# Kernel tuning notes

Hardware: AMD Instinct MI355X
Metric: run time of the kernel (lower is better)

## Reference

```python
import jax, jax.numpy as jnp
import numpy as np

BS, L, E, H, T, V = 1024, 128, 256, 512, 20, 1000


def setup_inputs() -> dict:
    key = jax.random.key(0)
    ks = jax.random.split(key, 16)
    s = 0.05
    msg = jax.random.randint(ks[0], (BS, T), 1, V + 1)
    M = jax.random.normal(ks[1], (BS, L, E), dtype=jnp.float32)
    input_mask = jax.random.randint(ks[2], (BS, L), 0, 2) == 1
    input_mask = input_mask.at[:, 0].set(False)  # guarantee >=1 unmasked slot
    lengths = jax.random.randint(ks[3], (BS,), 0, T + 1)
    emb = jax.random.normal(ks[4], (V + 1, E), dtype=jnp.float32) * s
    Wq = jax.random.normal(ks[5], (E, H), dtype=jnp.float32) * s   # query_projection
    bq = jnp.zeros((E,), dtype=jnp.float32)
    Wc = jax.random.normal(ks[6], (H, E + H), dtype=jnp.float32) * s  # attn_combine
    bc = jnp.zeros((H,), dtype=jnp.float32)
    W_ih = jax.random.normal(ks[7], (4 * H, E), dtype=jnp.float32) * s
    W_hh = jax.random.normal(ks[8], (4 * H, H), dtype=jnp.float32) * s
    b_ih = jnp.zeros((4 * H,), dtype=jnp.float32)
    b_hh = jnp.zeros((4 * H,), dtype=jnp.float32)
    return {"msg": msg, "M": M, "input_mask": input_mask, "lengths": lengths,
            "emb": emb, "Wq": Wq, "bq": bq, "Wc": Wc, "bc": bc,
            "W_ih": W_ih, "W_hh": W_hh, "b_ih": b_ih, "b_hh": b_hh}


def _attend(h, M, input_mask, Wq, bq, Wc, bc):
    # q=(bs,H) projected to key space (bs,E); scores over L objects
    pq = h @ Wq.T + bq                                   # (bs, E)
    scores = jnp.einsum('ble,be->bl', M, pq)             # (bs, L)
    scores = jnp.where(input_mask, -jnp.inf, scores)
    w = jax.nn.softmax(scores, axis=1)                   # (bs, L)
    applied = jnp.einsum('bl,ble->be', w, M)             # (bs, E)
    att_out = jnp.concatenate([applied, h], axis=1) @ Wc.T + bc  # (bs, H)
    return att_out, w


def _lstm_cell(x, h, c, W_ih, W_hh, b_ih, b_hh):
    gates = x @ W_ih.T + b_ih + h @ W_hh.T + b_hh        # (bs, 4H)
    i, f, g, o = jnp.split(gates, 4, axis=1)
    c_new = jax.nn.sigmoid(f) * c + jax.nn.sigmoid(i) * jnp.tanh(g)
    h_new = jax.nn.sigmoid(o) * jnp.tanh(c_new)
    return h_new, c_new


def reference(msg, M, input_mask, lengths, emb, Wq, bq, Wc, bc, W_ih, W_hh, b_ih, b_hh):
    bs = msg.shape[0]
    msg_embed = emb[msg]                                 # (bs, T, E)
    xs = jnp.swapaxes(msg_embed, 0, 1)                   # (T, bs, E)
    h0 = jnp.zeros((bs, H), dtype=M.dtype)
    c0 = jnp.zeros((bs, H), dtype=M.dtype)

    def step(carry, x):
        h, c = carry
        att_out, w = _attend(h, M, input_mask, Wq, bq, Wc, bc)
        h2, c2 = _lstm_cell(x, att_out, c, W_ih, W_hh, b_ih, b_hh)
        return (h2, c2), w

    (hT, _), ws = jax.lax.scan(step, (h0, c0), xs)       # ws: (T, bs, L)
    _, w_last = _attend(hT, M, input_mask, Wq, bq, Wc, bc)
    attn_weights = jnp.swapaxes(jnp.concatenate([ws, w_last[None]], axis=0), 0, 1)  # (bs, T+1, L)
    lengths_c = jnp.clip(lengths, 0, T)
    output = attn_weights[jnp.arange(bs), lengths_c]     # (bs, L)
    logits = jnp.zeros((bs,), dtype=M.dtype)
    entropy = logits
    return (output, logits, entropy)
```

## Files before the change

kernel.cpp:

```cpp
#include <hip/hip_runtime.h>
#include <math.h>

#define NB 1024
#define L_ 128
#define E_ 256
#define H_ 512
#define T_ 20
#define CH 32
#define NCH 4

typedef _Float16 h8 __attribute__((ext_vector_type(8)));
typedef float f4 __attribute__((ext_vector_type(4)));

__global__ __launch_bounds__(256) void detect_mask(const unsigned char* __restrict__ mask,
                                                   int* __restrict__ flag) {
    int i = blockIdx.x * 256 + threadIdx.x;
    if (mask[4 * i + 1] != 0) flag[0] = 1;
}

__global__ __launch_bounds__(256) void attend_part(
    const float* __restrict__ M, const unsigned char* __restrict__ maskB,
    const int* __restrict__ flag, const float* __restrict__ pq,
    float* __restrict__ pbuf,
    float* __restrict__ apart,
    float2* __restrict__ stats)
{
    const int s = blockIdx.x, b = blockIdx.y;
    const int tid = threadIdx.x;
    __shared__ float pq_s[E_];
    __shared__ float ps[CH];

    pq_s[tid] = pq[b * E_ + tid];
    __syncthreads();

    const int wave = tid >> 6, lane = tid & 63;
    const int r = lane >> 3, i = lane & 7;
    const int l = wave * 8 + r;
    const float* Mrow = M + ((size_t)b * L_ + s * CH + l) * E_;

    float acc = 0.f;
    #pragma unroll
    for (int j = 0; j < 8; ++j) {
        float4 mv = *reinterpret_cast<const float4*>(Mrow + i * 4 + j * 32);
        float4 pv = *reinterpret_cast<const float4*>(pq_s + i * 4 + j * 32);
        acc += mv.x * pv.x + mv.y * pv.y + mv.z * pv.z + mv.w * pv.w;
    }
    acc += __shfl_down(acc, 4, 64);
    acc += __shfl_down(acc, 2, 64);
    acc += __shfl_down(acc, 1, 64);

    __shared__ float sc[CH];
    if (i == 0) {
        const int lg = s * CH + l;
        int msk = flag[0] ? (int)maskB[b * L_ + lg] : ((const int*)maskB)[b * L_ + lg];
        sc[l] = msk ? -INFINITY : acc;
    }
    __syncthreads();

    if (wave == 0) {
        const float v = (lane < CH) ? sc[lane] : -INFINITY;
        float m = v;
        #pragma unroll
        for (int off = 32; off > 0; off >>= 1) m = fmaxf(m, __shfl_down(m, off, 64));
        m = __shfl(m, 0, 64);
        const float p = (lane < CH && !isinf(m)) ? __expf(v - m) : 0.f;
        float ss = p;
        #pragma unroll
        for (int off = 32; off > 0; off >>= 1) ss += __shfl_down(ss, off, 64);
        if (lane == 0) stats[b * NCH + s] = make_float2(m, ss);
        if (lane < CH) {
            ps[lane] = p;
            pbuf[b * L_ + s * CH + lane] = p;
        }
    }
    __syncthreads();

    const float* Mc = M + ((size_t)b * L_ + s * CH) * E_;
    float a = 0.f;
    #pragma unroll 8
    for (int l2 = 0; l2 < CH; ++l2) a += ps[l2] * Mc[l2 * E_ + tid];
    apart[((size_t)b * NCH + s) * E_ + tid] = a;
}

__global__ __launch_bounds__(256) void attend_combine(
    const float* __restrict__ pbuf, const float* __restrict__ apart,
    const float2* __restrict__ stats, const int* __restrict__ lengths,
    float* __restrict__ applied, float* __restrict__ out, int t, int writeApplied)
{
    const int b = blockIdx.x;
    const int tid = threadIdx.x;
    __shared__ float scale[NCH];
    __shared__ float zinv;

    if (tid == 0) {
        float m = -INFINITY;
        #pragma unroll
        for (int s = 0; s < NCH; ++s) m = fmaxf(m, stats[b * NCH + s].x);
        float Z = 0.f;
        #pragma unroll
        for (int s = 0; s < NCH; ++s) {
            const float2 st = stats[b * NCH + s];
            const float sc = isinf(st.x) ? 0.f : __expf(st.x - m);
            scale[s] = sc;
            Z += st.y * sc;
        }
        zinv = 1.f / Z;
    }
    __syncthreads();

    if (writeApplied) {
        float a = 0.f;
        #pragma unroll
        for (int s = 0; s < NCH; ++s)
            a += apart[((size_t)b * NCH + s) * E_ + tid] * scale[s];
        applied[b * E_ + tid] = a * zinv;
    }

    int lc = lengths[b];
    lc = lc < 0 ? 0 : (lc > T_ ? T_ : lc);
    if (lc == t && tid < L_)
        out[(size_t)b * L_ + tid] = pbuf[b * L_ + tid] * scale[tid >> 5] * zinv;
}

__device__ inline void cvt8(const float4& x0, const float4& x1, h8& hi, h8& lo) {
    float xs[8] = {x0.x, x0.y, x0.z, x0.w, x1.x, x1.y, x1.z, x1.w};
    #pragma unroll
    for (int e = 0; e < 8; ++e) {
        _Float16 hh = (_Float16)xs[e];
        hi[e] = hh;
        lo[e] = (_Float16)((xs[e] - (float)hh) * 2048.0f);
    }
}

__global__ __launch_bounds__(256) void gemm_hilo(
    const float* __restrict__ A1, const float* __restrict__ A2, int K1,
    const int* __restrict__ gidx, int t,
    const float* __restrict__ B1, const float* __restrict__ B2, int BK1,
    const float* __restrict__ bias, float* __restrict__ C, int Nn, int Kn)
{
    __shared__ __align__(16) _Float16 Ah[64][40];
    __shared__ __align__(16) _Float16 Al[64][40];
    __shared__ __align__(16) _Float16 Bh[64][40];
    __shared__ __align__(16) _Float16 Bl[64][40];

    const int tid = threadIdx.x;
    const int n0 = blockIdx.x * 64, m0 = blockIdx.y * 64;
    const int lane = tid & 63, wv = tid >> 6;
    const int wr = (wv >> 1) * 32, wc = (wv & 1) * 32;
    const int fr = lane & 15, kg = (lane >> 4) * 8;
    const int sr = tid >> 2, skq = (tid & 3) * 8;

    f4 acc1[2][2] = {};
    f4 acc2[2][2] = {};
    const int KnmK1 = Kn - K1;
    const int KnmB  = Kn - BK1;

    for (int k0 = 0; k0 < Kn; k0 += 32) {
        {
            const int k = k0 + skq;
            const float* src;
            if (k < K1) {
                const int rr = gidx ? gidx[(m0 + sr) * T_ + t] : (m0 + sr);
                src = A1 + (size_t)rr * K1 + k;
            } else {
                src = A2 + (size_t)(m0 + sr) * KnmK1 + (k - K1);
            }
            float4 x0 = *reinterpret_cast<const float4*>(src);
            float4 x1 = *reinterpret_cast<const float4*>(src + 4);
            h8 hi, lo;
            cvt8(x0, x1, hi, lo);
            *reinterpret_cast<h8*>(&Ah[sr][skq]) = hi;
            *reinterpret_cast<h8*>(&Al[sr][skq]) = lo;
        }
        {
            const int k = k0 + skq;
            const float* src;
            if (k < BK1) src = B1 + (size_t)(n0 + sr) * BK1 + k;
            else         src = B2 + (size_t)(n0 + sr) * KnmB + (k - BK1);
            float4 x0 = *reinterpret_cast<const float4*>(src);
            float4 x1 = *reinterpret_cast<const float4*>(src + 4);
            h8 hi, lo;
            cvt8(x0, x1, hi, lo);
            *reinterpret_cast<h8*>(&Bh[sr][skq]) = hi;
            *reinterpret_cast<h8*>(&Bl[sr][skq]) = lo;
        }
        __syncthreads();

        h8 ah[2], al[2], bh[2], bl[2];
        #pragma unroll
        for (int i = 0; i < 2; ++i) {
            ah[i] = *reinterpret_cast<const h8*>(&Ah[wr + i * 16 + fr][kg]);
            al[i] = *reinterpret_cast<const h8*>(&Al[wr + i * 16 + fr][kg]);
            bh[i] = *reinterpret_cast<const h8*>(&Bh[wc + i * 16 + fr][kg]);
            bl[i] = *reinterpret_cast<const h8*>(&Bl[wc + i * 16 + fr][kg]);
        }
        #pragma unroll
        for (int i = 0; i < 2; ++i)
            #pragma unroll
            for (int j = 0; j < 2; ++j) {
                acc1[i][j] = __builtin_amdgcn_mfma_f32_16x16x32_f16(ah[i], bh[j], acc1[i][j], 0, 0, 0);
                acc2[i][j] = __builtin_amdgcn_mfma_f32_16x16x32_f16(ah[i], bl[j], acc2[i][j], 0, 0, 0);
                acc2[i][j] = __builtin_amdgcn_mfma_f32_16x16x32_f16(al[i], bh[j], acc2[i][j], 0, 0, 0);
            }
        __syncthreads();
    }

    const int crow0 = m0 + wr + (lane >> 4) * 4;
    const int ccol0 = n0 + wc + fr;
    #pragma unroll
    for (int i = 0; i < 2; ++i)
        #pragma unroll
        for (int j = 0; j < 2; ++j) {
            const int col = ccol0 + j * 16;
            const float bv = bias[col];
            #pragma unroll
            for (int r = 0; r < 4; ++r) {
                const int row = crow0 + i * 16 + r;
                C[(size_t)row * Nn + col] =
                    acc1[i][j][r] + acc2[i][j][r] * (1.0f / 2048.0f) + bv;
            }
        }
}

__global__ __launch_bounds__(256) void lstm_cell(
    const float* __restrict__ gates, const float* __restrict__ b_hh,
    float* __restrict__ h, float* __restrict__ c)
{
    const int idx = blockIdx.x * 256 + threadIdx.x;
    const int b = idx >> 7, q = (idx & 127) * 4;
    const float* gb = gates + (size_t)b * 2048;
    const float4 gi = *reinterpret_cast<const float4*>(gb + q);
    const float4 gf = *reinterpret_cast<const float4*>(gb + 512 + q);
    const float4 gg = *reinterpret_cast<const float4*>(gb + 1024 + q);
    const float4 go = *reinterpret_cast<const float4*>(gb + 1536 + q);
    const float4 bi = *reinterpret_cast<const float4*>(b_hh + q);
    const float4 bf = *reinterpret_cast<const float4*>(b_hh + 512 + q);
    const float4 bg = *reinterpret_cast<const float4*>(b_hh + 1024 + q);
    const float4 bo = *reinterpret_cast<const float4*>(b_hh + 1536 + q);
    const size_t hidx = (size_t)b * H_ + q;
    float4 cv = *reinterpret_cast<const float4*>(c + hidx);
    float4 hn, cn;
    const float* pi = (const float*)&gi; const float* pf = (const float*)&gf;
    const float* pg = (const float*)&gg; const float* po = (const float*)&go;
    const float* qi = (const float*)&bi; const float* qf = (const float*)&bf;
    const float* qg = (const float*)&bg; const float* qo = (const float*)&bo;
    float* pc = (float*)&cv; float* oc = (float*)&cn; float* oh = (float*)&hn;
    #pragma unroll
    for (int e = 0; e < 4; ++e) {
        const float vi = pi[e] + qi[e], vf = pf[e] + qf[e];
        const float vg = pg[e] + qg[e], vo = po[e] + qo[e];
        const float si = 1.0f / (1.0f + __expf(-vi));
        const float sf = 1.0f / (1.0f + __expf(-vf));
        const float so = 1.0f / (1.0f + __expf(-vo));
        const float tg = tanhf(vg);
        const float cnew = sf * pc[e] + si * tg;
        oc[e] = cnew;
        oh[e] = so * tanhf(cnew);
    }
    *reinterpret_cast<float4*>(c + hidx) = cn;
    *reinterpret_cast<float4*>(h + hidx) = hn;
}

extern "C" void kernel_launch(void* const* d_in, const int* in_sizes, int n_in,
                              void* d_out, int out_size, void* d_ws, size_t ws_size,
                              hipStream_t stream)
{
    const int*   msg     = (const int*)d_in[0];
    const float* M       = (const float*)d_in[1];
    const unsigned char* mask = (const unsigned char*)d_in[2];
    const int*   lengths = (const int*)d_in[3];
    const float* emb     = (const float*)d_in[4];
    const float* Wq      = (const float*)d_in[5];
    const float* bq      = (const float*)d_in[6];
    const float* Wc      = (const float*)d_in[7];
    const float* bc      = (const float*)d_in[8];
    const float* W_ih    = (const float*)d_in[9];
    const float* W_hh    = (const float*)d_in[10];
    const float* b_ih    = (const float*)d_in[11];
    const float* b_hh    = (const float*)d_in[12];
    float* out = (float*)d_out;

    float*  ws      = (float*)d_ws;
    float*  h       = ws;
    float*  c       = ws + 524288;
    float*  pq      = ws + 1048576;
    float*  applied = ws + 1310720;
    float*  att     = ws + 1572864;
    float*  gates   = ws + 2097152;
    int*    flag    = (int*)(ws + 4194304);
    float*  pbuf    = ws + 4194560;
    float*  apart   = ws + 4325632;
    float2* stats   = (float2*)(ws + 5374208);

    hipMemsetAsync(h, 0, 524288 * 4, stream);
    hipMemsetAsync(c, 0, 524288 * 4, stream);
    hipMemsetAsync(flag, 0, 4, stream);
    hipMemsetAsync(out + (size_t)NB * L_, 0, 2 * NB * 4, stream);

    detect_mask<<<128, 256, 0, stream>>>(mask, flag);

    for (int t = 0; t < T_; ++t) {
        gemm_hilo<<<dim3(4, 16), 256, 0, stream>>>(
            h, h, 512, nullptr, 0, Wq, Wq, 512, bq, pq, 256, 512);
        attend_part<<<dim3(NCH, NB), 256, 0, stream>>>(
            M, mask, flag, pq, pbuf, apart, stats);
        attend_combine<<<NB, 256, 0, stream>>>(
            pbuf, apart, stats, lengths, applied, out, t, 1);
        gemm_hilo<<<dim3(8, 16), 256, 0, stream>>>(
            applied, h, 256, nullptr, 0, Wc, Wc, 768, bc, att, 512, 768);
        gemm_hilo<<<dim3(32, 16), 256, 0, stream>>>(
            emb, att, 256, msg, t, W_ih, W_hh, 256, b_ih, gates, 2048, 768);
        lstm_cell<<<512, 256, 0, stream>>>(gates, b_hh, h, c);
    }
    gemm_hilo<<<dim3(4, 16), 256, 0, stream>>>(
        h, h, 512, nullptr, 0, Wq, Wq, 512, bq, pq, 256, 512);
    attend_part<<<dim3(NCH, NB), 256, 0, stream>>>(
        M, mask, flag, pq, pbuf, apart, stats);
    attend_combine<<<NB, 256, 0, stream>>>(
        pbuf, apart, stats, lengths, applied, out, T_, 0);
}
```

Baseline: 2.436 ms.

## Pre-split weights and activations into fp16 hi/lo once instead of per-tile

Weights (Wq, Wc, embedding, concatenated W_ih/W_hh) are converted once per call into fp16 hi/lo pairs. Producers (attend_combine, the Wc GEMM epilogue, lstm_cell) now write activations directly in hi/lo fp16 form. The GEMM loads fp16 tiles straight into shared memory, which removes repeated fp32 loads and per-tile conversion work inside every timestep. In exchange it adds four setup conversion kernels and extra workspace, and the epilogue writes carry runtime branches on null pointers.

```diff
diff --git a/kernel.cpp b/kernel.cpp
--- a/kernel.cpp
+++ b/kernel.cpp
@@ -10,12 +10,37 @@
 #define NCH 4
 
 typedef _Float16 h8 __attribute__((ext_vector_type(8)));
+typedef _Float16 h4 __attribute__((ext_vector_type(4)));
 typedef float f4 __attribute__((ext_vector_type(4)));
 
 __global__ __launch_bounds__(256) void detect_mask(const unsigned char* __restrict__ mask,
                                                    int* __restrict__ flag) {
     int i = blockIdx.x * 256 + threadIdx.x;
     if (mask[4 * i + 1] != 0) flag[0] = 1;
+}
+
+__global__ __launch_bounds__(256) void split_plain(const float* __restrict__ src,
+                                                   _Float16* __restrict__ dh,
+                                                   _Float16* __restrict__ dl, int n) {
+    int i = blockIdx.x * 256 + threadIdx.x;
+    if (i < n) {
+        float x = src[i];
+        _Float16 hh = (_Float16)x;
+        dh[i] = hh;
+        dl[i] = (_Float16)((x - (float)hh) * 2048.0f);
+    }
+}
+
+__global__ __launch_bounds__(256) void split_concat(const float* __restrict__ Wih,
+                                                    const float* __restrict__ Whh,
+                                                    _Float16* __restrict__ dh,
+                                                    _Float16* __restrict__ dl) {
+    int i = blockIdx.x * 256 + threadIdx.x;
+    int r = i / 768, k = i - r * 768;
+    float x = (k < 256) ? Wih[r * 256 + k] : Whh[r * 512 + (k - 256)];
+    _Float16 hh = (_Float16)x;
+    dh[i] = hh;
+    dl[i] = (_Float16)((x - (float)hh) * 2048.0f);
 }
 
 __global__ __launch_bounds__(256) void attend_part(
@@ -85,7 +110,8 @@
 __global__ __launch_bounds__(256) void attend_combine(
     const float* __restrict__ pbuf, const float* __restrict__ apart,
     const float2* __restrict__ stats, const int* __restrict__ lengths,
-    float* __restrict__ applied, float* __restrict__ out, int t, int writeApplied)
+    _Float16* __restrict__ ap_h, _Float16* __restrict__ ap_l,
+    float* __restrict__ out, int t, int writeApplied)
 {
     const int b = blockIdx.x;
     const int tid = threadIdx.x;
@@ -113,7 +139,10 @@
         #pragma unroll
         for (int s = 0; s < NCH; ++s)
             a += apart[((size_t)b * NCH + s) * E_ + tid] * scale[s];
-        applied[b * E_ + tid] = a * zinv;
+        a *= zinv;
+        _Float16 hh = (_Float16)a;
+        ap_h[b * E_ + tid] = hh;
+        ap_l[b * E_ + tid] = (_Float16)((a - (float)hh) * 2048.0f);
     }
 
     int lc = lengths[b];
@@ -122,26 +151,19 @@
         out[(size_t)b * L_ + tid] = pbuf[b * L_ + tid] * scale[tid >> 5] * zinv;
 }
 
-__device__ inline void cvt8(const float4& x0, const float4& x1, h8& hi, h8& lo) {
-    float xs[8] = {x0.x, x0.y, x0.z, x0.w, x1.x, x1.y, x1.z, x1.w};
-    #pragma unroll
-    for (int e = 0; e < 8; ++e) {
-        _Float16 hh = (_Float16)xs[e];
-        hi[e] = hh;
-        lo[e] = (_Float16)((xs[e] - (float)hh) * 2048.0f);
-    }
-}
-
-__global__ __launch_bounds__(256) void gemm_hilo(
-    const float* __restrict__ A1, const float* __restrict__ A2, int K1,
+__global__ __launch_bounds__(256) void gemm_f16(
+    const _Float16* __restrict__ A1h, const _Float16* __restrict__ A1l, int K1,
     const int* __restrict__ gidx, int t,
-    const float* __restrict__ B1, const float* __restrict__ B2, int BK1,
-    const float* __restrict__ bias, float* __restrict__ C, int Nn, int Kn)
-{
-    __shared__ __align__(16) _Float16 Ah[64][40];
-    __shared__ __align__(16) _Float16 Al[64][40];
-    __shared__ __align__(16) _Float16 Bh[64][40];
-    __shared__ __align__(16) _Float16 Bl[64][40];
+    const _Float16* __restrict__ A2h, const _Float16* __restrict__ A2l,
+    const _Float16* __restrict__ Bh, const _Float16* __restrict__ Bl,
+    const float* __restrict__ bias, float* __restrict__ Cf,
+    _Float16* __restrict__ Ch, _Float16* __restrict__ Cl,
+    int Nn, int Kn)
+{
+    __shared__ __align__(16) _Float16 Ah_s[64][40];
+    __shared__ __align__(16) _Float16 Al_s[64][40];
+    __shared__ __align__(16) _Float16 Bh_s[64][40];
+    __shared__ __align__(16) _Float16 Bl_s[64][40];
 
     const int tid = threadIdx.x;
     const int n0 = blockIdx.x * 64, m0 = blockIdx.y * 64;
@@ -153,46 +175,33 @@
     f4 acc1[2][2] = {};
     f4 acc2[2][2] = {};
     const int KnmK1 = Kn - K1;
-    const int KnmB  = Kn - BK1;
 
     for (int k0 = 0; k0 < Kn; k0 += 32) {
-        {
-            const int k = k0 + skq;
-            const float* src;
-            if (k < K1) {
-                const int rr = gidx ? gidx[(m0 + sr) * T_ + t] : (m0 + sr);
-                src = A1 + (size_t)rr * K1 + k;
-            } else {
-                src = A2 + (size_t)(m0 + sr) * KnmK1 + (k - K1);
-            }
-            float4 x0 = *reinterpret_cast<const float4*>(src);
-            float4 x1 = *reinterpret_cast<const float4*>(src + 4);
-            h8 hi, lo;
-            cvt8(x0, x1, hi, lo);
-            *reinterpret_cast<h8*>(&Ah[sr][skq]) = hi;
-            *reinterpret_cast<h8*>(&Al[sr][skq]) = lo;
-        }
-        {
-            const int k = k0 + skq;
-            const float* src;
-            if (k < BK1) src = B1 + (size_t)(n0 + sr) * BK1 + k;
-            else         src = B2 + (size_t)(n0 + sr) * KnmB + (k - BK1);
-            float4 x0 = *reinterpret_cast<const float4*>(src);
-            float4 x1 = *reinterpret_cast<const float4*>(src + 4);
-            h8 hi, lo;
-            cvt8(x0, x1, hi, lo);
-            *reinterpret_cast<h8*>(&Bh[sr][skq]) = hi;
-            *reinterpret_cast<h8*>(&Bl[sr][skq]) = lo;
-        }
+        const int k = k0 + skq;
+        const _Float16 *sh, *sl;
+        if (k < K1) {
+            const int rr = gidx ? gidx[(m0 + sr) * T_ + t] : (m0 + sr);
+            sh = A1h + (size_t)rr * K1 + k;
+            sl = A1l + (size_t)rr * K1 + k;
+        } else {
+            sh = A2h + (size_t)(m0 + sr) * KnmK1 + (k - K1);
+            sl = A2l + (size_t)(m0 + sr) * KnmK1 + (k - K1);
+        }
+        *reinterpret_cast<h8*>(&Ah_s[sr][skq]) = *reinterpret_cast<const h8*>(sh);
+        *reinterpret_cast<h8*>(&Al_s[sr][skq]) = *reinterpret_cast<const h8*>(sl);
+        const _Float16* bp = Bh + (size_t)(n0 + sr) * Kn + k;
+        const _Float16* blp = Bl + (size_t)(n0 + sr) * Kn + k;
+        *reinterpret_cast<h8*>(&Bh_s[sr][skq]) = *reinterpret_cast<const h8*>(bp);
+        *reinterpret_cast<h8*>(&Bl_s[sr][skq]) = *reinterpret_cast<const h8*>(blp);
         __syncthreads();
 
         h8 ah[2], al[2], bh[2], bl[2];
         #pragma unroll
         for (int i = 0; i < 2; ++i) {
-            ah[i] = *reinterpret_cast<const h8*>(&Ah[wr + i * 16 + fr][kg]);
-            al[i] = *reinterpret_cast<const h8*>(&Al[wr + i * 16 + fr][kg]);
-            bh[i] = *reinterpret_cast<const h8*>(&Bh[wc + i * 16 + fr][kg]);
-            bl[i] = *reinterpret_cast<const h8*>(&Bl[wc + i * 16 + fr][kg]);
+            ah[i] = *reinterpret_cast<const h8*>(&Ah_s[wr + i * 16 + fr][kg]);
+            al[i] = *reinterpret_cast<const h8*>(&Al_s[wr + i * 16 + fr][kg]);
+            bh[i] = *reinterpret_cast<const h8*>(&Bh_s[wc + i * 16 + fr][kg]);
+            bl[i] = *reinterpret_cast<const h8*>(&Bl_s[wc + i * 16 + fr][kg]);
         }
         #pragma unroll
         for (int i = 0; i < 2; ++i)
@@ -216,15 +225,22 @@
             #pragma unroll
             for (int r = 0; r < 4; ++r) {
                 const int row = crow0 + i * 16 + r;
-                C[(size_t)row * Nn + col] =
-                    acc1[i][j][r] + acc2[i][j][r] * (1.0f / 2048.0f) + bv;
+                const float v = acc1[i][j][r] + acc2[i][j][r] * (1.0f / 2048.0f) + bv;
+                const size_t idx = (size_t)row * Nn + col;
+                if (Cf) Cf[idx] = v;
+                if (Ch) {
+                    _Float16 hh = (_Float16)v;
+                    Ch[idx] = hh;
+                    Cl[idx] = (_Float16)((v - (float)hh) * 2048.0f);
+                }
             }
         }
 }
 
 __global__ __launch_bounds__(256) void lstm_cell(
     const float* __restrict__ gates, const float* __restrict__ b_hh,
-    float* __restrict__ h, float* __restrict__ c)
+    _Float16* __restrict__ h_h, _Float16* __restrict__ h_l,
+    float* __restrict__ c)
 {
     const int idx = blockIdx.x * 256 + threadIdx.x;
     const int b = idx >> 7, q = (idx & 127) * 4;
@@ -239,12 +255,13 @@
     const float4 bo = *reinterpret_cast<const float4*>(b_hh + 1536 + q);
     const size_t hidx = (size_t)b * H_ + q;
     float4 cv = *reinterpret_cast<const float4*>(c + hidx);
-    float4 hn, cn;
+    float4 cn;
+    h4 hh_v, hl_v;
     const float* pi = (const float*)&gi; const float* pf = (const float*)&gf;
     const float* pg = (const float*)&gg; const float* po = (const float*)&go;
     const float* qi = (const float*)&bi; const float* qf = (const float*)&bf;
     const float* qg = (const float*)&bg; const float* qo = (const float*)&bo;
-    float* pc = (float*)&cv; float* oc = (float*)&cn; float* oh = (float*)&hn;
+    float* pc = (float*)&cv; float* oc = (float*)&cn;
     #pragma unroll
     for (int e = 0; e < 4; ++e) {
         const float vi = pi[e] + qi[e], vf = pf[e] + qf[e];
@@ -255,10 +272,14 @@
         const float tg = tanhf(vg);
         const float cnew = sf * pc[e] + si * tg;
         oc[e] = cnew;
-        oh[e] = so * tanhf(cnew);
+        const float hn = so * tanhf(cnew);
+        _Float16 hh = (_Float16)hn;
+        hh_v[e] = hh;
+        hl_v[e] = (_Float16)((hn - (float)hh) * 2048.0f);
     }
     *reinterpret_cast<float4*>(c + hidx) = cn;
-    *reinterpret_cast<float4*>(h + hidx) = hn;
+    *reinterpret_cast<h4*>(h_h + hidx) = hh_v;
+    *reinterpret_cast<h4*>(h_l + hidx) = hl_v;
 }
 
 extern "C" void kernel_launch(void* const* d_in, const int* in_sizes, int n_in,
@@ -280,42 +301,64 @@
     const float* b_hh    = (const float*)d_in[12];
     float* out = (float*)d_out;
 
-    float*  ws      = (float*)d_ws;
-    float*  h       = ws;
-    float*  c       = ws + 524288;
-    float*  pq      = ws + 1048576;
-    float*  applied = ws + 1310720;
-    float*  att     = ws + 1572864;
-    float*  gates   = ws + 2097152;
-    int*    flag    = (int*)(ws + 4194304);
-    float*  pbuf    = ws + 4194560;
-    float*  apart   = ws + 4325632;
-    float2* stats   = (float2*)(ws + 5374208);
-
-    hipMemsetAsync(h, 0, 524288 * 4, stream);
+    float*  ws    = (float*)d_ws;
+    float*  c     = ws;
+    float*  pq    = ws + 524288;
+    float*  gates = ws + 786432;
+    float*  pbuf  = ws + 2883584;
+    float*  apart = ws + 3014656;
+    float2* stats = (float2*)(ws + 4063232);
+    int*    flag  = (int*)(ws + 4071424);
+
+    _Float16* f16b = (_Float16*)(ws + 4071680);
+    _Float16* h_h  = f16b;
+    _Float16* h_l  = f16b + 524288;
+    _Float16* ap_h = f16b + 1048576;
+    _Float16* ap_l = f16b + 1310720;
+    _Float16* at_h = f16b + 1572864;
+    _Float16* at_l = f16b + 2097152;
+    _Float16* em_h = f16b + 2621440;
+    _Float16* em_l = f16b + 2877696;
+    _Float16* Wq_h = f16b + 3133952;
+    _Float16* Wq_l = f16b + 3265024;
+    _Float16* Wc_h = f16b + 3396096;
+    _Float16* Wc_l = f16b + 3789312;
+    _Float16* Wg_h = f16b + 4182528;
+    _Float16* Wg_l = f16b + 5755392;
+
     hipMemsetAsync(c, 0, 524288 * 4, stream);
+    hipMemsetAsync(h_h, 0, 524288 * 2, stream);
+    hipMemsetAsync(h_l, 0, 524288 * 2, stream);
     hipMemsetAsync(flag, 0, 4, stream);
     hipMemsetAsync(out + (size_t)NB * L_, 0, 2 * NB * 4, stream);
 
     detect_mask<<<128, 256, 0, stream>>>(mask, flag);
+    split_plain<<<512, 256, 0, stream>>>(Wq, Wq_h, Wq_l, 131072);
+    split_plain<<<1536, 256, 0, stream>>>(Wc, Wc_h, Wc_l, 393216);
+    split_plain<<<1001, 256, 0, stream>>>(emb, em_h, em_l, 256256);
+    split_concat<<<6144, 256, 0, stream>>>(W_ih, W_hh, Wg_h, Wg_l);
 
     for (int t = 0; t < T_; ++t) {
-        gemm_hilo<<<dim3(4, 16), 256, 0, stream>>>(
-            h, h, 512, nullptr, 0, Wq, Wq, 512, bq, pq, 256, 512);
+        gemm_f16<<<dim3(4, 16), 256, 0, stream>>>(
+            h_h, h_l, 512, nullptr, 0, h_h, h_l, Wq_h, Wq_l,
+            bq, pq, nullptr, nullptr, 256, 512);
         attend_part<<<dim3(NCH, NB), 256, 0, stream>>>(
             M, mask, flag, pq, pbuf, apart, stats);
         attend_combine<<<NB, 256, 0, stream>>>(
-            pbuf, apart, stats, lengths, applied, out, t, 1);
-        gemm_hilo<<<dim3(8, 16), 256, 0, stream>>>(
-            applied, h, 256, nullptr, 0, Wc, Wc, 768, bc, att, 512, 768);
-        gemm_hilo<<<dim3(32, 16), 256, 0, stream>>>(
-            emb, att, 256, msg, t, W_ih, W_hh, 256, b_ih, gates, 2048, 768);
-        lstm_cell<<<512, 256, 0, stream>>>(gates, b_hh, h, c);
-    }
-    gemm_hilo<<<dim3(4, 16), 256, 0, stream>>>(
-        h, h, 512, nullptr, 0, Wq, Wq, 512, bq, pq, 256, 512);
+            pbuf, apart, stats, lengths, ap_h, ap_l, out, t, 1);
+        gemm_f16<<<dim3(8, 16), 256, 0, stream>>>(
+            ap_h, ap_l, 256, nullptr, 0, h_h, h_l, Wc_h, Wc_l,
+            bc, nullptr, at_h, at_l, 512, 768);
+        gemm_f16<<<dim3(32, 16), 256, 0, stream>>>(
+            em_h, em_l, 256, msg, t, at_h, at_l, Wg_h, Wg_l,
+            b_ih, gates, nullptr, nullptr, 2048, 768);
+        lstm_cell<<<512, 256, 0, stream>>>(gates, b_hh, h_h, h_l, c);
+    }
+    gemm_f16<<<dim3(4, 16), 256, 0, stream>>>(
+        h_h, h_l, 512, nullptr, 0, h_h, h_l, Wq_h, Wq_l,
+        bq, pq, nullptr, nullptr, 256, 512);
     attend_part<<<dim3(NCH, NB), 256, 0, stream>>>(
         M, mask, flag, pq, pbuf, apart, stats);
     attend_combine<<<NB, 256, 0, stream>>>(
-        pbuf, apart, stats, lengths, applied, out, T_, 0);
-}
+        pbuf, apart, stats, lengths, ap_h, ap_l, out, T_, 0);
+}
```

After: 2.295 ms. -5.8%, faster.
